# Performance work log

Hardware: AMD Instinct MI355X
Metric: run time of the kernel (lower is better)

The kernel has to match this reference:

```python
import jax, jax.numpy as jnp
import numpy as np

NEG_SLOPE = 0.2  # PyG GATConv default


def _gat_layer(x, src, dst, W, a_s, a_d, b, num_nodes):
    H, C = a_s.shape
    h = (x @ W).reshape(num_nodes, H, C)                     # [N,H,C]
    alpha_src = jnp.einsum('nhc,hc->nh', h, a_s)             # [N,H]
    alpha_dst = jnp.einsum('nhc,hc->nh', h, a_d)             # [N,H]
    e = jax.nn.leaky_relu(alpha_src[src] + alpha_dst[dst], NEG_SLOPE)  # [E,H]
    # segment softmax over incoming edges of each destination node
    m = jax.lax.stop_gradient(jax.ops.segment_max(e, dst, num_segments=num_nodes))
    e = jnp.exp(e - m[dst])
    den = jax.ops.segment_sum(e, dst, num_segments=num_nodes)
    alpha = e / den[dst]                                     # [E,H]
    msg = h[src] * alpha[:, :, None]                         # [E,H,C]
    out = jax.ops.segment_sum(msg, dst, num_segments=num_nodes)
    return out.reshape(num_nodes, H * C) + b


def setup_inputs() -> dict:
    key = jax.random.key(0)
    ks = jax.random.split(key, 10)
    N, E, D, H, C = 100000, 1600000, 128, 4, 32
    s = 1.0 / np.sqrt(D)
    return {
        'x': jax.random.normal(ks[0], (N, D), jnp.float32),
        'edge_index': jax.random.randint(ks[1], (2, E), 0, N, jnp.int64),
        'W1': jax.random.normal(ks[2], (D, H * C), jnp.float32) * s,
        'a_src1': jax.random.normal(ks[3], (H, C), jnp.float32) * s,
        'a_dst1': jax.random.normal(ks[4], (H, C), jnp.float32) * s,
        'b1': jnp.zeros((H * C,), jnp.float32),
        'W2': jax.random.normal(ks[5], (H * C, H * C), jnp.float32) * s,
        'a_src2': jax.random.normal(ks[6], (H, C), jnp.float32) * s,
        'a_dst2': jax.random.normal(ks[7], (H, C), jnp.float32) * s,
        'b2': jnp.zeros((H * C,), jnp.float32),
    }


def reference(x, edge_index, W1, a_src1, a_dst1, b1, W2, a_src2, a_dst2, b2):
    N = x.shape[0]
    loop = jnp.arange(N, dtype=edge_index.dtype)  # PyG add_self_loops=True
    src = jnp.concatenate([edge_index[0], loop])
    dst = jnp.concatenate([edge_index[1], loop])
    h = _gat_layer(x, src, dst, W1, a_src1, a_dst1, b1, N)
    h = jax.nn.relu(h)
    h = _gat_layer(h, src, dst, W2, a_src2, a_dst2, b2, N)
    return jax.nn.relu(h)
```

## Files before the change

kernel.cpp:

```cpp
#include <hip/hip_runtime.h>
#include <cstdint>
#include <cstddef>

#define NEG_SLOPE 0.2f
#define BIN_SHIFT 9
#define BCAP 16384
#define LOG2E 1.4426950408889634f

typedef short bf16x8 __attribute__((ext_vector_type(8)));
typedef float f32x4 __attribute__((ext_vector_type(4)));

#if __has_builtin(__builtin_amdgcn_exp2f)
#define EXP2(x) __builtin_amdgcn_exp2f(x)
#else
#define EXP2(x) exp2f(x)
#endif

static __device__ __forceinline__ unsigned short bf16r(float f) {
    unsigned u = __float_as_uint(f);
    return (unsigned short)((u + 0x7fffu + ((u >> 16) & 1u)) >> 16);
}
static __device__ __forceinline__ float bfu_lo(unsigned u) { return __uint_as_float(u << 16); }
static __device__ __forceinline__ float bfu_hi(unsigned u) { return __uint_as_float(u & 0xffff0000u); }

__global__ __launch_bounds__(256) void wprep_k(const float* __restrict__ W1, const float* __restrict__ W2,
                                               unsigned short* __restrict__ Wh1, unsigned short* __restrict__ Wl1,
                                               unsigned short* __restrict__ Wh2, unsigned short* __restrict__ Wl2,
                                               int* __restrict__ bcnt) {
    if (blockIdx.x == 0) bcnt[threadIdx.x] = 0;
    int t = blockIdx.x * 256 + threadIdx.x;
    const float* W;
    unsigned short *Wh, *Wl;
    int idx;
    if (t < 16384) { W = W1; Wh = Wh1; Wl = Wl1; idx = t; }
    else           { W = W2; Wh = Wh2; Wl = Wl2; idx = t - 16384; }
    int c = idx >> 7;
    int k = idx & 127;
    float w = W[(size_t)k * 128 + c];
    unsigned short h = bf16r(w);
    float lo = w - __uint_as_float((unsigned)h << 16);
    int dst = (k >> 5) * 4096 + (c >> 4) * 512 + (((k >> 3) & 3) * 16 + (c & 15)) * 8 + (k & 7);
    Wh[dst] = h;
    Wl[dst] = bf16r(lo);
}

__global__ __launch_bounds__(256) void bin_k(const int* __restrict__ srcI, const int* __restrict__ dstI,
                                             int E, int N, int K, int* __restrict__ bcnt,
                                             int* __restrict__ tmpE) {
    __shared__ int hist[256];
    __shared__ int lbase[256];
    __shared__ int lstart[256];
    __shared__ int cur[256];
    __shared__ int sc[256];
    __shared__ int staged[4096];
    __shared__ unsigned char bs[4096];
    const int t = threadIdx.x;
    const int M = E + N;
    const int chunk0 = blockIdx.x * 4096;
    hist[t] = 0;
    __syncthreads();

    int pk[16], bk[16];
#pragma unroll
    for (int j = 0; j < 16; ++j) {
        int i = chunk0 + t + j * 256;
        bk[j] = -1;
        if (i < M) {
            int ss, dd;
            if (i < E) { ss = srcI[i]; dd = dstI[i]; }
            else       { ss = i - E;  dd = ss; }
            if ((unsigned)dd < (unsigned)N && (unsigned)ss < (unsigned)N) {
                bk[j] = dd >> BIN_SHIFT;
                pk[j] = (ss << 9) | (dd & 511);
                atomicAdd(&hist[bk[j]], 1);
            }
        }
    }
    __syncthreads();
    const int h = hist[t];
    lbase[t] = (h > 0) ? atomicAdd(&bcnt[t], h) : 0;
    sc[t] = h;
    __syncthreads();
    for (int off = 1; off < 256; off <<= 1) {
        int v = (t >= off) ? sc[t - off] : 0;
        __syncthreads();
        sc[t] += v;
        __syncthreads();
    }
    lstart[t] = sc[t] - h;
    cur[t]    = sc[t] - h;
    __syncthreads();
#pragma unroll
    for (int j = 0; j < 16; ++j) {
        if (bk[j] >= 0) {
            int r = atomicAdd(&cur[bk[j]], 1);
            staged[r] = pk[j];
            bs[r] = (unsigned char)bk[j];
        }
    }
    const int total = sc[255];
    __syncthreads();
    for (int s = t; s < total; s += 256) {
        int b = bs[s];
        int posInBucket = lbase[b] + (s - lstart[b]);
        if (posInBucket < BCAP) tmpE[(size_t)b * BCAP + posInBucket] = staged[s];
    }
}

__global__ __launch_bounds__(256) void scatter_csr_k(const int* __restrict__ tmpE,
                                                     const int* __restrict__ bcnt,
                                                     int* __restrict__ rowptr,
                                                     int* __restrict__ colOff,
                                                     int N, int K) {
    __shared__ int pre[256];
    __shared__ int cur[512];
    __shared__ int ss[256];
    const int t = threadIdx.x;
    const int b = blockIdx.x;

    int bc = (t < K) ? min(bcnt[t], BCAP) : 0;
    pre[t] = bc;
    __syncthreads();
    for (int off = 1; off < 256; off <<= 1) {
        int v = (t >= off) ? pre[t - off] : 0;
        __syncthreads();
        pre[t] += v;
        __syncthreads();
    }
    const int base_b = (b == 0) ? 0 : pre[b - 1];
    const int cnt_b  = pre[b] - base_b;
    if (b == K - 1 && t == 0) rowptr[N] = pre[K - 1];

    const int nlo = b << BIN_SHIFT;
    const int nhi = min(nlo + (1 << BIN_SHIFT), N);
    const int nn  = nhi - nlo;
    const int* te = tmpE + (size_t)b * BCAP;

    cur[t] = 0;
    cur[t + 256] = 0;
    __syncthreads();
    for (int i = t; i < cnt_b; i += 256) atomicAdd(&cur[te[i] & 511], 1);
    __syncthreads();

    int v0 = cur[2 * t], v1 = cur[2 * t + 1];
    ss[t] = v0 + v1;
    __syncthreads();
    for (int off = 1; off < 256; off <<= 1) {
        int v = (t >= off) ? ss[t - off] : 0;
        __syncthreads();
        ss[t] += v;
        __syncthreads();
    }
    int e0 = (t == 0) ? 0 : ss[t - 1];
    int e1 = e0 + v0;
    if (2 * t < nn)     rowptr[nlo + 2 * t]     = base_b + e0;
    if (2 * t + 1 < nn) rowptr[nlo + 2 * t + 1] = base_b + e1;
    cur[2 * t] = e0;
    cur[2 * t + 1] = e1;
    __syncthreads();

    for (int i = t; i < cnt_b; i += 256) {
        int v = te[i];
        int r = atomicAdd(&cur[v & 511], 1);
        colOff[base_b + r] = ((unsigned)v >> 9) << 8;
    }
}

__global__ __launch_bounds__(256) void gemm_mfma_k(const float* __restrict__ X,
                                                   const unsigned short* __restrict__ Wh,
                                                   const unsigned short* __restrict__ Wl,
                                                   const float* __restrict__ a_s,
                                                   const float* __restrict__ a_d,
                                                   unsigned short* __restrict__ Hout,
                                                   float* __restrict__ asrc,
                                                   float* __restrict__ adst,
                                                   int N) {
    __shared__ __align__(16) unsigned short hstage[4][32][132];
    const int tid = threadIdx.x;
    const int wid = tid >> 6;
    const int l   = tid & 63;
    const int l15 = l & 15;
    const int lh  = l >> 4;
    const int waveRow = blockIdx.x * 128 + wid * 32;
    if (waveRow >= N) return;

    f32x4 acc[2][8];
#pragma unroll
    for (int m = 0; m < 2; ++m)
#pragma unroll
        for (int f = 0; f < 8; ++f)
#pragma unroll
            for (int c = 0; c < 4; ++c) acc[m][f][c] = 0.f;

    const int r0 = waveRow + l15;
    const int r1 = waveRow + 16 + l15;
    const size_t xoff0 = (size_t)min(r0, N - 1) * 128;
    const size_t xoff1 = (size_t)min(r1, N - 1) * 128;
    const int kb = lh * 8;

#pragma unroll
    for (int ks = 0; ks < 4; ++ks) {
        bf16x8 ah[2], al[2];
#pragma unroll
        for (int m = 0; m < 2; ++m) {
            const float* xp = X + (m ? xoff1 : xoff0) + ks * 32 + kb;
            float4 v0 = *(const float4*)xp;
            float4 v1 = *(const float4*)(xp + 4);
            float xs[8] = {v0.x, v0.y, v0.z, v0.w, v1.x, v1.y, v1.z, v1.w};
#pragma unroll
            for (int j = 0; j < 8; ++j) {
                unsigned short h = bf16r(xs[j]);
                float hf = __uint_as_float((unsigned)h << 16);
                ah[m][j] = (short)h;
                al[m][j] = (short)bf16r(xs[j] - hf);
            }
        }
        const unsigned short* wbh = Wh + ks * 4096 + l * 8;
        const unsigned short* wbl = Wl + ks * 4096 + l * 8;
#pragma unroll
        for (int f = 0; f < 8; ++f) {
            bf16x8 wh = *(const bf16x8*)(wbh + f * 512);
            bf16x8 wl = *(const bf16x8*)(wbl + f * 512);
#pragma unroll
            for (int m = 0; m < 2; ++m) {
                acc[m][f] = __builtin_amdgcn_mfma_f32_16x16x32_bf16(ah[m], wh, acc[m][f], 0, 0, 0);
                acc[m][f] = __builtin_amdgcn_mfma_f32_16x16x32_bf16(al[m], wh, acc[m][f], 0, 0, 0);
                acc[m][f] = __builtin_amdgcn_mfma_f32_16x16x32_bf16(ah[m], wl, acc[m][f], 0, 0, 0);
            }
        }
    }

    float asf[8], adf[8];
#pragma unroll
    for (int f = 0; f < 8; ++f) {
        asf[f] = a_s[f * 16 + l15];
        adf[f] = a_d[f * 16 + l15];
    }
    const int q = l15;
#pragma unroll
    for (int m = 0; m < 2; ++m) {
#pragma unroll
        for (int r = 0; r < 4; ++r) {
            float ps[4] = {0.f, 0.f, 0.f, 0.f};
            float pd[4] = {0.f, 0.f, 0.f, 0.f};
#pragma unroll
            for (int f = 0; f < 8; ++f) {
                float v = acc[m][f][r];
                ps[f >> 1] = fmaf(v, asf[f], ps[f >> 1]);
                pd[f >> 1] = fmaf(v, adf[f], pd[f >> 1]);
                hstage[wid][m * 16 + lh * 4 + r][f * 16 + l15] = bf16r(v);
            }
#pragma unroll
            for (int mask = 1; mask < 16; mask <<= 1) {
#pragma unroll
                for (int h = 0; h < 4; ++h) {
                    ps[h] += __shfl_xor(ps[h], mask);
                    pd[h] += __shfl_xor(pd[h], mask);
                }
            }
            int row = waveRow + m * 16 + lh * 4 + r;
            if (q < 8 && row < N) {
                float v0 = (q & 1) ? ps[1] : ps[0];
                float v1 = (q & 1) ? ps[3] : ps[2];
                float vs = (q & 2) ? v1 : v0;
                float w0 = (q & 1) ? pd[1] : pd[0];
                float w1 = (q & 1) ? pd[3] : pd[2];
                float vd = (q & 2) ? w1 : w0;
                if (q < 4) asrc[row * 4 + q] = vs * LOG2E;
                else       adst[row * 4 + (q - 4)] = vd * LOG2E;
            }
        }
    }

#pragma unroll
    for (int it = 0; it < 8; ++it) {
        int row = it * 4 + lh;
        const unsigned short* hp = &hstage[wid][row][l15 * 8];
        uint2 aa = *(const uint2*)hp;
        uint2 bb = *(const uint2*)(hp + 4);
        int grow = waveRow + row;
        if (grow < N) {
            uint4 o;
            o.x = aa.x; o.y = aa.y; o.z = bb.x; o.w = bb.y;
            *(uint4*)&Hout[(size_t)grow * 128 + l15 * 8] = o;
        }
    }
}

__global__ __launch_bounds__(256) void aggregate_k(const unsigned short* __restrict__ Hbuf,
                                                   const float* __restrict__ asrc,
                                                   const float* __restrict__ adst,
                                                   const int* __restrict__ rowptr,
                                                   const int* __restrict__ colOff,
                                                   const float* __restrict__ bias,
                                                   float* __restrict__ out, int N) {
    int wave = (blockIdx.x * 256 + threadIdx.x) >> 6;
    int lane = threadIdx.x & 63;
    if (wave >= N) return;
    const int n = wave;
    const int c0 = lane * 2;
    const int head = c0 >> 5;
    const float adh = adst[n * 4 + head];
    const char* Hb = (const char*)Hbuf;
    const char* As = (const char*)asrc;
    const int hoff = c0 * 2;
    const int aoff = head * 4;

    int b = __builtin_amdgcn_readfirstlane(rowptr[n]);
    int e = __builtin_amdgcn_readfirstlane(rowptr[n + 1]);
    float acc0 = 0.f, acc1 = 0.f, sw = 0.f;
    for (int p = b; p < e; p += 8) {
        int off[8];
#pragma unroll
        for (int j = 0; j < 8; ++j) off[j] = colOff[min(p + j, e - 1)];
        float a[8];
#pragma unroll
        for (int j = 0; j < 8; ++j) a[j] = *(const float*)(As + (off[j] >> 4) + aoff);
        unsigned hu[8];
#pragma unroll
        for (int j = 0; j < 8; ++j) hu[j] = *(const unsigned*)(Hb + off[j] + hoff);
#pragma unroll
        for (int j = 0; j < 8; ++j) {
            float x = a[j] + adh;
            float w = (p + j < e) ? EXP2(fmaxf(x, NEG_SLOPE * x)) : 0.f;
            sw += w;
            acc0 = fmaf(w, bfu_lo(hu[j]), acc0);
            acc1 = fmaf(w, bfu_hi(hu[j]), acc1);
        }
    }
    float inv = 1.f / sw;
    float o0 = fmaxf(acc0 * inv + bias[c0], 0.f);
    float o1 = fmaxf(acc1 * inv + bias[c0 + 1], 0.f);
    *(float2*)&out[(size_t)n * 128 + c0] = make_float2(o0, o1);
}


extern "C" void kernel_launch(void* const* d_in, const int* in_sizes, int n_in,
                              void* d_out, int out_size, void* d_ws, size_t ws_size,
                              hipStream_t stream) {
    const float* X   = (const float*)d_in[0];
    const int*   EI  = (const int*)d_in[1];
    const float* W1  = (const float*)d_in[2];
    const float* as1 = (const float*)d_in[3];
    const float* ad1 = (const float*)d_in[4];
    const float* b1  = (const float*)d_in[5];
    const float* W2  = (const float*)d_in[6];
    const float* as2 = (const float*)d_in[7];
    const float* ad2 = (const float*)d_in[8];
    const float* b2  = (const float*)d_in[9];

    const int N = in_sizes[0] / 128;
    const int E = in_sizes[1] / 2;
    const int M = E + N;
    const int K = (N + (1 << BIN_SHIFT) - 1) >> BIN_SHIFT;
    const int* srcI = EI;
    const int* dstI = EI + E;

    char* w = (char*)d_ws;
    auto alloc = [&](size_t bytes) {
        char* p = w;
        w += (bytes + 255) & ~(size_t)255;
        return p;
    };
    unsigned short* Hbuf = (unsigned short*)alloc((size_t)N * 128 * 2);
    float* asrc   = (float*)alloc((size_t)N * 4 * 4);
    float* adst   = (float*)alloc((size_t)N * 4 * 4);
    int*   rowptr = (int*)alloc((size_t)(N + 1) * 4);
    int*   colOff = (int*)alloc((size_t)M * 4);
    int*   tmpE   = (int*)alloc((size_t)K * BCAP * 4);
    int*   bcnt   = (int*)alloc(256 * 4);
    unsigned short* Wt1h = (unsigned short*)alloc(128 * 128 * 2);
    unsigned short* Wt1l = (unsigned short*)alloc(128 * 128 * 2);
    unsigned short* Wt2h = (unsigned short*)alloc(128 * 128 * 2);
    unsigned short* Wt2l = (unsigned short*)alloc(128 * 128 * 2);

    const int gemmBlocks = (N + 127) / 128;
    float* out = (float*)d_out;

    wprep_k<<<128, 256, 0, stream>>>(W1, W2, Wt1h, Wt1l, Wt2h, Wt2l, bcnt);
    bin_k<<<(M + 4095) / 4096, 256, 0, stream>>>(srcI, dstI, E, N, K, bcnt, tmpE);
    scatter_csr_k<<<K, 256, 0, stream>>>(tmpE, bcnt, rowptr, colOff, N, K);
    gemm_mfma_k<<<gemmBlocks, 256, 0, stream>>>(X, Wt1h, Wt1l, as1, ad1, Hbuf, asrc, adst, N);
    aggregate_k<<<((size_t)N * 64 + 255) / 256, 256, 0, stream>>>(Hbuf, asrc, adst, rowptr, colOff, b1, out, N);
    gemm_mfma_k<<<gemmBlocks, 256, 0, stream>>>(out, Wt2h, Wt2l, as2, ad2, Hbuf, asrc, adst, N);
    aggregate_k<<<((size_t)N * 64 + 255) / 256, 256, 0, stream>>>(Hbuf, asrc, adst, rowptr, colOff, b2, out, N);
}
```

Baseline: 378.3 us.

## Fuse pipeline stages into two persistent cooperative kernels with grid syncs

Replaces the seven separate launches with two cooperative persistent kernels. One does weight prep, binning and CSR scatter; the other does both GEMM and aggregation layers. Grid-wide syncs and threadfences replace kernel boundaries. This removes launch gaps and per-kernel tail effects, but the fixed grid size and the occupancy hint of 3 blocks per unit may lower parallelism or occupancy for the latency-bound aggregation. Grid-stride loops and the original multi-launch path are kept as a fallback if the cooperative launch fails.

```diff
diff --git a/kernel.cpp b/kernel.cpp
--- a/kernel.cpp
+++ b/kernel.cpp
@@ -1,6 +1,9 @@
 #include <hip/hip_runtime.h>
+#include <hip/hip_cooperative_groups.h>
 #include <cstdint>
 #include <cstddef>
+
+namespace cg = cooperative_groups;
 
 #define NEG_SLOPE 0.2f
 #define BIN_SHIFT 9
@@ -23,12 +26,10 @@
 static __device__ __forceinline__ float bfu_lo(unsigned u) { return __uint_as_float(u << 16); }
 static __device__ __forceinline__ float bfu_hi(unsigned u) { return __uint_as_float(u & 0xffff0000u); }
 
-__global__ __launch_bounds__(256) void wprep_k(const float* __restrict__ W1, const float* __restrict__ W2,
-                                               unsigned short* __restrict__ Wh1, unsigned short* __restrict__ Wl1,
-                                               unsigned short* __restrict__ Wh2, unsigned short* __restrict__ Wl2,
-                                               int* __restrict__ bcnt) {
-    if (blockIdx.x == 0) bcnt[threadIdx.x] = 0;
-    int t = blockIdx.x * 256 + threadIdx.x;
+
+static __device__ __forceinline__ void wprep_elem(int t, const float* W1, const float* W2,
+                                                  unsigned short* Wh1, unsigned short* Wl1,
+                                                  unsigned short* Wh2, unsigned short* Wl2) {
     const float* W;
     unsigned short *Wh, *Wl;
     int idx;
@@ -44,19 +45,13 @@
     Wl[dst] = bf16r(lo);
 }
 
-__global__ __launch_bounds__(256) void bin_k(const int* __restrict__ srcI, const int* __restrict__ dstI,
-                                             int E, int N, int K, int* __restrict__ bcnt,
-                                             int* __restrict__ tmpE) {
-    __shared__ int hist[256];
-    __shared__ int lbase[256];
-    __shared__ int lstart[256];
-    __shared__ int cur[256];
-    __shared__ int sc[256];
-    __shared__ int staged[4096];
-    __shared__ unsigned char bs[4096];
+static __device__ void bin_body(int bid, const int* __restrict__ srcI, const int* __restrict__ dstI,
+                                int E, int N, int K, int* __restrict__ bcnt, int* __restrict__ tmpE,
+                                int* hist, int* lbase, int* lstart, int* cur, int* sc,
+                                int* staged, unsigned char* bs) {
     const int t = threadIdx.x;
     const int M = E + N;
-    const int chunk0 = blockIdx.x * 4096;
+    const int chunk0 = bid * 4096;
     hist[t] = 0;
     __syncthreads();
 
@@ -105,18 +100,13 @@
         int posInBucket = lbase[b] + (s - lstart[b]);
         if (posInBucket < BCAP) tmpE[(size_t)b * BCAP + posInBucket] = staged[s];
     }
-}
-
-__global__ __launch_bounds__(256) void scatter_csr_k(const int* __restrict__ tmpE,
-                                                     const int* __restrict__ bcnt,
-                                                     int* __restrict__ rowptr,
-                                                     int* __restrict__ colOff,
-                                                     int N, int K) {
-    __shared__ int pre[256];
-    __shared__ int cur[512];
-    __shared__ int ss[256];
+    __syncthreads();
+}
+
+static __device__ void scatter_body(int b, const int* __restrict__ tmpE, const int* __restrict__ bcnt,
+                                    int* __restrict__ rowptr, int* __restrict__ colOff,
+                                    int N, int K, int* pre, int* cur, int* ss) {
     const int t = threadIdx.x;
-    const int b = blockIdx.x;
 
     int bc = (t < K) ? min(bcnt[t], BCAP) : 0;
     pre[t] = bc;
@@ -164,24 +154,24 @@
         int r = atomicAdd(&cur[v & 511], 1);
         colOff[base_b + r] = ((unsigned)v >> 9) << 8;
     }
-}
-
-__global__ __launch_bounds__(256) void gemm_mfma_k(const float* __restrict__ X,
-                                                   const unsigned short* __restrict__ Wh,
-                                                   const unsigned short* __restrict__ Wl,
-                                                   const float* __restrict__ a_s,
-                                                   const float* __restrict__ a_d,
-                                                   unsigned short* __restrict__ Hout,
-                                                   float* __restrict__ asrc,
-                                                   float* __restrict__ adst,
-                                                   int N) {
-    __shared__ __align__(16) unsigned short hstage[4][32][132];
+    __syncthreads();
+}
+
+static __device__ void gemm_body(int bid, const float* __restrict__ X,
+                                 const unsigned short* __restrict__ Wh,
+                                 const unsigned short* __restrict__ Wl,
+                                 const float* __restrict__ a_s,
+                                 const float* __restrict__ a_d,
+                                 unsigned short* __restrict__ Hout,
+                                 float* __restrict__ asrc,
+                                 float* __restrict__ adst,
+                                 int N, unsigned short* hstage) {
     const int tid = threadIdx.x;
     const int wid = tid >> 6;
     const int l   = tid & 63;
     const int l15 = l & 15;
     const int lh  = l >> 4;
-    const int waveRow = blockIdx.x * 128 + wid * 32;
+    const int waveRow = bid * 128 + wid * 32;
     if (waveRow >= N) return;
 
     f32x4 acc[2][8];
@@ -248,7 +238,7 @@
                 float v = acc[m][f][r];
                 ps[f >> 1] = fmaf(v, asf[f], ps[f >> 1]);
                 pd[f >> 1] = fmaf(v, adf[f], pd[f >> 1]);
-                hstage[wid][m * 16 + lh * 4 + r][f * 16 + l15] = bf16r(v);
+                hstage[((wid * 32) + m * 16 + lh * 4 + r) * 132 + f * 16 + l15] = bf16r(v);
             }
 #pragma unroll
             for (int mask = 1; mask < 16; mask <<= 1) {
@@ -275,7 +265,7 @@
 #pragma unroll
     for (int it = 0; it < 8; ++it) {
         int row = it * 4 + lh;
-        const unsigned short* hp = &hstage[wid][row][l15 * 8];
+        const unsigned short* hp = hstage + ((wid * 32) + row) * 132 + l15 * 8;
         uint2 aa = *(const uint2*)hp;
         uint2 bb = *(const uint2*)(hp + 4);
         int grow = waveRow + row;
@@ -287,17 +277,14 @@
     }
 }
 
-__global__ __launch_bounds__(256) void aggregate_k(const unsigned short* __restrict__ Hbuf,
-                                                   const float* __restrict__ asrc,
-                                                   const float* __restrict__ adst,
-                                                   const int* __restrict__ rowptr,
-                                                   const int* __restrict__ colOff,
-                                                   const float* __restrict__ bias,
-                                                   float* __restrict__ out, int N) {
-    int wave = (blockIdx.x * 256 + threadIdx.x) >> 6;
-    int lane = threadIdx.x & 63;
-    if (wave >= N) return;
-    const int n = wave;
+static __device__ void agg_body(int grp, const unsigned short* __restrict__ Hbuf,
+                                const float* __restrict__ asrc, const float* __restrict__ adst,
+                                const int* __restrict__ rowptr, const int* __restrict__ colOff,
+                                const float* __restrict__ bias, float* __restrict__ out, int N) {
+    const int wid  = threadIdx.x >> 6;
+    const int lane = threadIdx.x & 63;
+    const int n = grp * 4 + wid;
+    if (n >= N) return;
     const int c0 = lane * 2;
     const int head = c0 >> 5;
     const float adh = adst[n * 4 + head];
@@ -332,6 +319,111 @@
     float o0 = fmaxf(acc0 * inv + bias[c0], 0.f);
     float o1 = fmaxf(acc1 * inv + bias[c0 + 1], 0.f);
     *(float2*)&out[(size_t)n * 128 + c0] = make_float2(o0, o1);
+}
+
+
+struct PrepArgs {
+    const float *W1, *W2;
+    unsigned short *Wh1, *Wl1, *Wh2, *Wl2;
+    int* bcnt;
+    const int *srcI, *dstI;
+    int* tmpE;
+    int *rowptr, *colOff;
+    int E, N, K, nchunks;
+};
+
+__global__ __launch_bounds__(256) void prep_coop_k(PrepArgs a) {
+    __shared__ int hist[256], lbase[256], lstart[256], curA[256], sc[256];
+    __shared__ int staged[4096];
+    __shared__ unsigned char bs[4096];
+    __shared__ int pre[256], curB[512], ss[256];
+    cg::grid_group grid = cg::this_grid();
+    const int t = threadIdx.x;
+
+    if (blockIdx.x == 0) a.bcnt[t] = 0;
+    for (int i = blockIdx.x * 256 + t; i < 32768; i += gridDim.x * 256)
+        wprep_elem(i, a.W1, a.W2, a.Wh1, a.Wl1, a.Wh2, a.Wl2);
+    __threadfence();
+    grid.sync();
+
+    for (int c = blockIdx.x; c < a.nchunks; c += gridDim.x)
+        bin_body(c, a.srcI, a.dstI, a.E, a.N, a.K, a.bcnt, a.tmpE,
+                 hist, lbase, lstart, curA, sc, staged, bs);
+    __threadfence();
+    grid.sync();
+
+    for (int b = blockIdx.x; b < a.K; b += gridDim.x)
+        scatter_body(b, a.tmpE, a.bcnt, a.rowptr, a.colOff, a.N, a.K, pre, curB, ss);
+}
+
+struct MainArgs {
+    const float* X;
+    const unsigned short *Wh1, *Wl1, *Wh2, *Wl2;
+    const float *as1, *ad1, *b1, *as2, *ad2, *b2;
+    unsigned short* Hbuf;
+    float *asrc, *adst;
+    const int *rowptr, *colOff;
+    float* out;
+    int N, gemmTiles, nodeGroups;
+};
+
+__global__ __launch_bounds__(256, 3) void main_coop_k(MainArgs a) {
+    __shared__ __align__(16) unsigned short hstage[4 * 32 * 132];
+    cg::grid_group grid = cg::this_grid();
+
+    for (int tl = blockIdx.x; tl < a.gemmTiles; tl += gridDim.x)
+        gemm_body(tl, a.X, a.Wh1, a.Wl1, a.as1, a.ad1, a.Hbuf, a.asrc, a.adst, a.N, hstage);
+    __threadfence();
+    grid.sync();
+    for (int gp = blockIdx.x; gp < a.nodeGroups; gp += gridDim.x)
+        agg_body(gp, a.Hbuf, a.asrc, a.adst, a.rowptr, a.colOff, a.b1, a.out, a.N);
+    __threadfence();
+    grid.sync();
+    for (int tl = blockIdx.x; tl < a.gemmTiles; tl += gridDim.x)
+        gemm_body(tl, a.out, a.Wh2, a.Wl2, a.as2, a.ad2, a.Hbuf, a.asrc, a.adst, a.N, hstage);
+    __threadfence();
+    grid.sync();
+    for (int gp = blockIdx.x; gp < a.nodeGroups; gp += gridDim.x)
+        agg_body(gp, a.Hbuf, a.asrc, a.adst, a.rowptr, a.colOff, a.b2, a.out, a.N);
+}
+
+
+__global__ __launch_bounds__(256) void wprep_k(const float* W1, const float* W2,
+                                               unsigned short* Wh1, unsigned short* Wl1,
+                                               unsigned short* Wh2, unsigned short* Wl2,
+                                               int* bcnt) {
+    if (blockIdx.x == 0) bcnt[threadIdx.x] = 0;
+    int t = blockIdx.x * 256 + threadIdx.x;
+    if (t < 32768) wprep_elem(t, W1, W2, Wh1, Wl1, Wh2, Wl2);
+}
+
+__global__ __launch_bounds__(256) void bin_k(const int* srcI, const int* dstI,
+                                             int E, int N, int K, int* bcnt, int* tmpE) {
+    __shared__ int hist[256], lbase[256], lstart[256], curA[256], sc[256];
+    __shared__ int staged[4096];
+    __shared__ unsigned char bs[4096];
+    bin_body(blockIdx.x, srcI, dstI, E, N, K, bcnt, tmpE, hist, lbase, lstart, curA, sc, staged, bs);
+}
+
+__global__ __launch_bounds__(256) void scatter_csr_k(const int* tmpE, const int* bcnt,
+                                                     int* rowptr, int* colOff, int N, int K) {
+    __shared__ int pre[256], curB[512], ss[256];
+    scatter_body(blockIdx.x, tmpE, bcnt, rowptr, colOff, N, K, pre, curB, ss);
+}
+
+__global__ __launch_bounds__(256) void gemm_mfma_k(const float* X, const unsigned short* Wh,
+                                                   const unsigned short* Wl, const float* a_s,
+                                                   const float* a_d, unsigned short* Hout,
+                                                   float* asrc, float* adst, int N) {
+    __shared__ __align__(16) unsigned short hstage[4 * 32 * 132];
+    gemm_body(blockIdx.x, X, Wh, Wl, a_s, a_d, Hout, asrc, adst, N, hstage);
+}
+
+__global__ __launch_bounds__(256) void aggregate_k(const unsigned short* Hbuf, const float* asrc,
+                                                   const float* adst, const int* rowptr,
+                                                   const int* colOff, const float* bias,
+                                                   float* out, int N) {
+    agg_body(blockIdx.x, Hbuf, asrc, adst, rowptr, colOff, bias, out, N);
 }
 
 
@@ -374,14 +466,70 @@
     unsigned short* Wt2h = (unsigned short*)alloc(128 * 128 * 2);
     unsigned short* Wt2l = (unsigned short*)alloc(128 * 128 * 2);
 
-    const int gemmBlocks = (N + 127) / 128;
+    const int gemmTiles  = (N + 127) / 128;
+    const int nodeGroups = (N + 3) / 4;
+    const int nchunks    = (M + 4095) / 4096;
     float* out = (float*)d_out;
 
-    wprep_k<<<128, 256, 0, stream>>>(W1, W2, Wt1h, Wt1l, Wt2h, Wt2l, bcnt);
-    bin_k<<<(M + 4095) / 4096, 256, 0, stream>>>(srcI, dstI, E, N, K, bcnt, tmpE);
-    scatter_csr_k<<<K, 256, 0, stream>>>(tmpE, bcnt, rowptr, colOff, N, K);
-    gemm_mfma_k<<<gemmBlocks, 256, 0, stream>>>(X, Wt1h, Wt1l, as1, ad1, Hbuf, asrc, adst, N);
-    aggregate_k<<<((size_t)N * 64 + 255) / 256, 256, 0, stream>>>(Hbuf, asrc, adst, rowptr, colOff, b1, out, N);
-    gemm_mfma_k<<<gemmBlocks, 256, 0, stream>>>(out, Wt2h, Wt2l, as2, ad2, Hbuf, asrc, adst, N);
-    aggregate_k<<<((size_t)N * 64 + 255) / 256, 256, 0, stream>>>(Hbuf, asrc, adst, rowptr, colOff, b2, out, N);
-}
+    static int s_numCU = 0, s_prepOcc = 0, s_mainOcc = 0;
+    if (s_numCU == 0) {
+        int dev = 0;
+        hipDeviceProp_t props;
+        if (hipGetDevice(&dev) == hipSuccess && hipGetDeviceProperties(&props, dev) == hipSuccess)
+            s_numCU = props.multiProcessorCount;
+        if (s_numCU <= 0) s_numCU = 256;
+        if (hipOccupancyMaxActiveBlocksPerMultiprocessor(&s_prepOcc, prep_coop_k, 256, 0) != hipSuccess)
+            s_prepOcc = 0;
+        if (hipOccupancyMaxActiveBlocksPerMultiprocessor(&s_mainOcc, main_coop_k, 256, 0) != hipSuccess)
+            s_mainOcc = 0;
+        (void)hipGetLastError();
+    }
+
+    bool prepDone = false, mainDone = false;
+
+    if (s_prepOcc > 0) {
+        int prepGrid = s_prepOcc * s_numCU;
+        if (prepGrid > nchunks) prepGrid = nchunks;
+        PrepArgs pa;
+        pa.W1 = W1; pa.W2 = W2;
+        pa.Wh1 = Wt1h; pa.Wl1 = Wt1l; pa.Wh2 = Wt2h; pa.Wl2 = Wt2l;
+        pa.bcnt = bcnt; pa.srcI = srcI; pa.dstI = dstI; pa.tmpE = tmpE;
+        pa.rowptr = rowptr; pa.colOff = colOff;
+        pa.E = E; pa.N = N; pa.K = K; pa.nchunks = nchunks;
+        void* pargs[] = { &pa };
+        if (hipLaunchCooperativeKernel(prep_coop_k, dim3(prepGrid), dim3(256), pargs, 0, stream) == hipSuccess)
+            prepDone = true;
+        else
+            (void)hipGetLastError();
+    }
+    if (!prepDone) {
+        wprep_k<<<128, 256, 0, stream>>>(W1, W2, Wt1h, Wt1l, Wt2h, Wt2l, bcnt);
+        bin_k<<<nchunks, 256, 0, stream>>>(srcI, dstI, E, N, K, bcnt, tmpE);
+        scatter_csr_k<<<K, 256, 0, stream>>>(tmpE, bcnt, rowptr, colOff, N, K);
+    }
+
+    if (s_mainOcc > 0) {
+        int mainGrid = s_mainOcc * s_numCU;
+        if (mainGrid > nodeGroups) mainGrid = nodeGroups;
+        MainArgs ma;
+        ma.X = X;
+        ma.Wh1 = Wt1h; ma.Wl1 = Wt1l; ma.Wh2 = Wt2h; ma.Wl2 = Wt2l;
+        ma.as1 = as1; ma.ad1 = ad1; ma.b1 = b1;
+        ma.as2 = as2; ma.ad2 = ad2; ma.b2 = b2;
+        ma.Hbuf = Hbuf; ma.asrc = asrc; ma.adst = adst;
+        ma.rowptr = rowptr; ma.colOff = colOff;
+        ma.out = out;
+        ma.N = N; ma.gemmTiles = gemmTiles; ma.nodeGroups = nodeGroups;
+        void* margs[] = { &ma };
+        if (hipLaunchCooperativeKernel(main_coop_k, dim3(mainGrid), dim3(256), margs, 0, stream) == hipSuccess)
+            mainDone = true;
+        else
+            (void)hipGetLastError();
+    }
+    if (!mainDone) {
+        gemm_mfma_k<<<gemmTiles, 256, 0, stream>>>(X, Wt1h, Wt1l, as1, ad1, Hbuf, asrc, adst, N);
+        aggregate_k<<<nodeGroups, 256, 0, stream>>>(Hbuf, asrc, adst, rowptr, colOff, b1, out, N);
+        gemm_mfma_k<<<gemmTiles, 256, 0, stream>>>(out, Wt2h, Wt2l, as2, ad2, Hbuf, asrc, adst, N);
+        aggregate_k<<<nodeGroups, 256, 0, stream>>>(Hbuf, asrc, adst, rowptr, colOff, b2, out, N);
+    }
+}
```

Measured after the change: 622.2 us. +64.5%, slower.

## Merge independent prep and layer-1 GEMM with CSR scatter into shared launches

Applied to the files above, without the earlier changes.

Weight preparation and edge binning now run as different block ranges of one kernel, and the CSR scatter runs alongside the first-layer GEMM in another combined kernel, since neither pair depends on the other. This removes two kernel launches and lets independent work overlap on the GPU. The bucket counter reset moves to a hipMemsetAsync. The combined kernels carry the larger shared-memory footprint and register use of their heavier half, which may lower occupancy for the lighter half.

```diff
diff --git a/kernel.cpp b/kernel.cpp
--- a/kernel.cpp
+++ b/kernel.cpp
@@ -23,12 +23,10 @@
 static __device__ __forceinline__ float bfu_lo(unsigned u) { return __uint_as_float(u << 16); }
 static __device__ __forceinline__ float bfu_hi(unsigned u) { return __uint_as_float(u & 0xffff0000u); }
 
-__global__ __launch_bounds__(256) void wprep_k(const float* __restrict__ W1, const float* __restrict__ W2,
-                                               unsigned short* __restrict__ Wh1, unsigned short* __restrict__ Wl1,
-                                               unsigned short* __restrict__ Wh2, unsigned short* __restrict__ Wl2,
-                                               int* __restrict__ bcnt) {
-    if (blockIdx.x == 0) bcnt[threadIdx.x] = 0;
-    int t = blockIdx.x * 256 + threadIdx.x;
+
+static __device__ __forceinline__ void wprep_elem(int t, const float* W1, const float* W2,
+                                                  unsigned short* Wh1, unsigned short* Wl1,
+                                                  unsigned short* Wh2, unsigned short* Wl2) {
     const float* W;
     unsigned short *Wh, *Wl;
     int idx;
@@ -44,19 +42,13 @@
     Wl[dst] = bf16r(lo);
 }
 
-__global__ __launch_bounds__(256) void bin_k(const int* __restrict__ srcI, const int* __restrict__ dstI,
-                                             int E, int N, int K, int* __restrict__ bcnt,
-                                             int* __restrict__ tmpE) {
-    __shared__ int hist[256];
-    __shared__ int lbase[256];
-    __shared__ int lstart[256];
-    __shared__ int cur[256];
-    __shared__ int sc[256];
-    __shared__ int staged[4096];
-    __shared__ unsigned char bs[4096];
+static __device__ void bin_body(int bid, const int* __restrict__ srcI, const int* __restrict__ dstI,
+                                int E, int N, int K, int* __restrict__ bcnt, int* __restrict__ tmpE,
+                                int* hist, int* lbase, int* lstart, int* cur, int* sc,
+                                int* staged, unsigned char* bs) {
     const int t = threadIdx.x;
     const int M = E + N;
-    const int chunk0 = blockIdx.x * 4096;
+    const int chunk0 = bid * 4096;
     hist[t] = 0;
     __syncthreads();
 
@@ -107,16 +99,10 @@
     }
 }
 
-__global__ __launch_bounds__(256) void scatter_csr_k(const int* __restrict__ tmpE,
-                                                     const int* __restrict__ bcnt,
-                                                     int* __restrict__ rowptr,
-                                                     int* __restrict__ colOff,
-                                                     int N, int K) {
-    __shared__ int pre[256];
-    __shared__ int cur[512];
-    __shared__ int ss[256];
+static __device__ void scatter_body(int b, const int* __restrict__ tmpE, const int* __restrict__ bcnt,
+                                    int* __restrict__ rowptr, int* __restrict__ colOff,
+                                    int N, int K, int* pre, int* cur, int* ss) {
     const int t = threadIdx.x;
-    const int b = blockIdx.x;
 
     int bc = (t < K) ? min(bcnt[t], BCAP) : 0;
     pre[t] = bc;
@@ -166,22 +152,21 @@
     }
 }
 
-__global__ __launch_bounds__(256) void gemm_mfma_k(const float* __restrict__ X,
-                                                   const unsigned short* __restrict__ Wh,
-                                                   const unsigned short* __restrict__ Wl,
-                                                   const float* __restrict__ a_s,
-                                                   const float* __restrict__ a_d,
-                                                   unsigned short* __restrict__ Hout,
-                                                   float* __restrict__ asrc,
-                                                   float* __restrict__ adst,
-                                                   int N) {
-    __shared__ __align__(16) unsigned short hstage[4][32][132];
+static __device__ void gemm_body(int bid, const float* __restrict__ X,
+                                 const unsigned short* __restrict__ Wh,
+                                 const unsigned short* __restrict__ Wl,
+                                 const float* __restrict__ a_s,
+                                 const float* __restrict__ a_d,
+                                 unsigned short* __restrict__ Hout,
+                                 float* __restrict__ asrc,
+                                 float* __restrict__ adst,
+                                 int N, unsigned short* hstage) {
     const int tid = threadIdx.x;
     const int wid = tid >> 6;
     const int l   = tid & 63;
     const int l15 = l & 15;
     const int lh  = l >> 4;
-    const int waveRow = blockIdx.x * 128 + wid * 32;
+    const int waveRow = bid * 128 + wid * 32;
     if (waveRow >= N) return;
 
     f32x4 acc[2][8];
@@ -248,7 +233,7 @@
                 float v = acc[m][f][r];
                 ps[f >> 1] = fmaf(v, asf[f], ps[f >> 1]);
                 pd[f >> 1] = fmaf(v, adf[f], pd[f >> 1]);
-                hstage[wid][m * 16 + lh * 4 + r][f * 16 + l15] = bf16r(v);
+                hstage[((wid * 32) + m * 16 + lh * 4 + r) * 132 + f * 16 + l15] = bf16r(v);
             }
 #pragma unroll
             for (int mask = 1; mask < 16; mask <<= 1) {
@@ -275,7 +260,7 @@
 #pragma unroll
     for (int it = 0; it < 8; ++it) {
         int row = it * 4 + lh;
-        const unsigned short* hp = &hstage[wid][row][l15 * 8];
+        const unsigned short* hp = hstage + ((wid * 32) + row) * 132 + l15 * 8;
         uint2 aa = *(const uint2*)hp;
         uint2 bb = *(const uint2*)(hp + 4);
         int grow = waveRow + row;
@@ -287,6 +272,109 @@
     }
 }
 
+static __device__ void agg_body(int grp, const unsigned short* __restrict__ Hbuf,
+                                const float* __restrict__ asrc, const float* __restrict__ adst,
+                                const int* __restrict__ rowptr, const int* __restrict__ colOff,
+                                const float* __restrict__ bias, float* __restrict__ out, int N) {
+    const int wid  = threadIdx.x >> 6;
+    const int lane = threadIdx.x & 63;
+    const int n = grp * 4 + wid;
+    if (n >= N) return;
+    const int c0 = lane * 2;
+    const int head = c0 >> 5;
+    const float adh = adst[n * 4 + head];
+    const char* Hb = (const char*)Hbuf;
+    const char* As = (const char*)asrc;
+    const int hoff = c0 * 2;
+    const int aoff = head * 4;
+
+    int b = __builtin_amdgcn_readfirstlane(rowptr[n]);
+    int e = __builtin_amdgcn_readfirstlane(rowptr[n + 1]);
+    float acc0 = 0.f, acc1 = 0.f, sw = 0.f;
+    for (int p = b; p < e; p += 8) {
+        int off[8];
+#pragma unroll
+        for (int j = 0; j < 8; ++j) off[j] = colOff[min(p + j, e - 1)];
+        float a[8];
+#pragma unroll
+        for (int j = 0; j < 8; ++j) a[j] = *(const float*)(As + (off[j] >> 4) + aoff);
+        unsigned hu[8];
+#pragma unroll
+        for (int j = 0; j < 8; ++j) hu[j] = *(const unsigned*)(Hb + off[j] + hoff);
+#pragma unroll
+        for (int j = 0; j < 8; ++j) {
+            float x = a[j] + adh;
+            float w = (p + j < e) ? EXP2(fmaxf(x, NEG_SLOPE * x)) : 0.f;
+            sw += w;
+            acc0 = fmaf(w, bfu_lo(hu[j]), acc0);
+            acc1 = fmaf(w, bfu_hi(hu[j]), acc1);
+        }
+    }
+    float inv = 1.f / sw;
+    float o0 = fmaxf(acc0 * inv + bias[c0], 0.f);
+    float o1 = fmaxf(acc1 * inv + bias[c0 + 1], 0.f);
+    *(float2*)&out[(size_t)n * 128 + c0] = make_float2(o0, o1);
+}
+
+
+__global__ __launch_bounds__(256) void prep1_k(const float* __restrict__ W1, const float* __restrict__ W2,
+                                               unsigned short* __restrict__ Wh1, unsigned short* __restrict__ Wl1,
+                                               unsigned short* __restrict__ Wh2, unsigned short* __restrict__ Wl2,
+                                               const int* __restrict__ srcI, const int* __restrict__ dstI,
+                                               int E, int N, int K, int* __restrict__ bcnt,
+                                               int* __restrict__ tmpE) {
+    __shared__ int hist[256], lbase[256], lstart[256], curA[256], sc[256];
+    __shared__ int staged[4096];
+    __shared__ unsigned char bs[4096];
+    const int bid = blockIdx.x;
+    if (bid < 128) {
+        int t = bid * 256 + threadIdx.x;
+        wprep_elem(t, W1, W2, Wh1, Wl1, Wh2, Wl2);
+    } else {
+        bin_body(bid - 128, srcI, dstI, E, N, K, bcnt, tmpE,
+                 hist, lbase, lstart, curA, sc, staged, bs);
+    }
+}
+
+__global__ __launch_bounds__(256) void gemm1_scatter_k(const int* __restrict__ tmpE,
+                                                       const int* __restrict__ bcnt,
+                                                       int* __restrict__ rowptr,
+                                                       int* __restrict__ colOff,
+                                                       int K,
+                                                       const float* __restrict__ X,
+                                                       const unsigned short* __restrict__ Wh,
+                                                       const unsigned short* __restrict__ Wl,
+                                                       const float* __restrict__ a_s,
+                                                       const float* __restrict__ a_d,
+                                                       unsigned short* __restrict__ Hout,
+                                                       float* __restrict__ asrc,
+                                                       float* __restrict__ adst,
+                                                       int N) {
+    __shared__ __align__(16) unsigned short smem[4 * 32 * 132];
+    const int bid = blockIdx.x;
+    if (bid < K) {
+        int* pre = (int*)smem;
+        int* cur = pre + 256;
+        int* ss  = cur + 512;
+        scatter_body(bid, tmpE, bcnt, rowptr, colOff, N, K, pre, cur, ss);
+    } else {
+        gemm_body(bid - K, X, Wh, Wl, a_s, a_d, Hout, asrc, adst, N, smem);
+    }
+}
+
+__global__ __launch_bounds__(256) void gemm_mfma_k(const float* __restrict__ X,
+                                                   const unsigned short* __restrict__ Wh,
+                                                   const unsigned short* __restrict__ Wl,
+                                                   const float* __restrict__ a_s,
+                                                   const float* __restrict__ a_d,
+                                                   unsigned short* __restrict__ Hout,
+                                                   float* __restrict__ asrc,
+                                                   float* __restrict__ adst,
+                                                   int N) {
+    __shared__ __align__(16) unsigned short hstage[4 * 32 * 132];
+    gemm_body(blockIdx.x, X, Wh, Wl, a_s, a_d, Hout, asrc, adst, N, hstage);
+}
+
 __global__ __launch_bounds__(256) void aggregate_k(const unsigned short* __restrict__ Hbuf,
                                                    const float* __restrict__ asrc,
                                                    const float* __restrict__ adst,
@@ -294,44 +382,7 @@
                                                    const int* __restrict__ colOff,
                                                    const float* __restrict__ bias,
                                                    float* __restrict__ out, int N) {
-    int wave = (blockIdx.x * 256 + threadIdx.x) >> 6;
-    int lane = threadIdx.x & 63;
-    if (wave >= N) return;
-    const int n = wave;
-    const int c0 = lane * 2;
-    const int head = c0 >> 5;
-    const float adh = adst[n * 4 + head];
-    const char* Hb = (const char*)Hbuf;
-    const char* As = (const char*)asrc;
-    const int hoff = c0 * 2;
-    const int aoff = head * 4;
-
-    int b = __builtin_amdgcn_readfirstlane(rowptr[n]);
-    int e = __builtin_amdgcn_readfirstlane(rowptr[n + 1]);
-    float acc0 = 0.f, acc1 = 0.f, sw = 0.f;
-    for (int p = b; p < e; p += 8) {
-        int off[8];
-#pragma unroll
-        for (int j = 0; j < 8; ++j) off[j] = colOff[min(p + j, e - 1)];
-        float a[8];
-#pragma unroll
-        for (int j = 0; j < 8; ++j) a[j] = *(const float*)(As + (off[j] >> 4) + aoff);
-        unsigned hu[8];
-#pragma unroll
-        for (int j = 0; j < 8; ++j) hu[j] = *(const unsigned*)(Hb + off[j] + hoff);
-#pragma unroll
-        for (int j = 0; j < 8; ++j) {
-            float x = a[j] + adh;
-            float w = (p + j < e) ? EXP2(fmaxf(x, NEG_SLOPE * x)) : 0.f;
-            sw += w;
-            acc0 = fmaf(w, bfu_lo(hu[j]), acc0);
-            acc1 = fmaf(w, bfu_hi(hu[j]), acc1);
-        }
-    }
-    float inv = 1.f / sw;
-    float o0 = fmaxf(acc0 * inv + bias[c0], 0.f);
-    float o1 = fmaxf(acc1 * inv + bias[c0 + 1], 0.f);
-    *(float2*)&out[(size_t)n * 128 + c0] = make_float2(o0, o1);
+    agg_body(blockIdx.x, Hbuf, asrc, adst, rowptr, colOff, bias, out, N);
 }
 
 
@@ -374,14 +425,17 @@
     unsigned short* Wt2h = (unsigned short*)alloc(128 * 128 * 2);
     unsigned short* Wt2l = (unsigned short*)alloc(128 * 128 * 2);
 
-    const int gemmBlocks = (N + 127) / 128;
+    const int gemmTiles  = (N + 127) / 128;
+    const int nodeGroups = (N + 3) / 4;
+    const int nchunks    = (M + 4095) / 4096;
     float* out = (float*)d_out;
 
-    wprep_k<<<128, 256, 0, stream>>>(W1, W2, Wt1h, Wt1l, Wt2h, Wt2l, bcnt);
-    bin_k<<<(M + 4095) / 4096, 256, 0, stream>>>(srcI, dstI, E, N, K, bcnt, tmpE);
-    scatter_csr_k<<<K, 256, 0, stream>>>(tmpE, bcnt, rowptr, colOff, N, K);
-    gemm_mfma_k<<<gemmBlocks, 256, 0, stream>>>(X, Wt1h, Wt1l, as1, ad1, Hbuf, asrc, adst, N);
-    aggregate_k<<<((size_t)N * 64 + 255) / 256, 256, 0, stream>>>(Hbuf, asrc, adst, rowptr, colOff, b1, out, N);
-    gemm_mfma_k<<<gemmBlocks, 256, 0, stream>>>(out, Wt2h, Wt2l, as2, ad2, Hbuf, asrc, adst, N);
-    aggregate_k<<<((size_t)N * 64 + 255) / 256, 256, 0, stream>>>(Hbuf, asrc, adst, rowptr, colOff, b2, out, N);
-}
+    hipMemsetAsync(bcnt, 0, 256 * 4, stream);
+    prep1_k<<<128 + nchunks, 256, 0, stream>>>(W1, W2, Wt1h, Wt1l, Wt2h, Wt2l,
+                                               srcI, dstI, E, N, K, bcnt, tmpE);
+    gemm1_scatter_k<<<K + gemmTiles, 256, 0, stream>>>(tmpE, bcnt, rowptr, colOff, K,
+                                                       X, Wt1h, Wt1l, as1, ad1, Hbuf, asrc, adst, N);
+    aggregate_k<<<nodeGroups, 256, 0, stream>>>(Hbuf, asrc, adst, rowptr, colOff, b1, out, N);
+    gemm_mfma_k<<<gemmTiles, 256, 0, stream>>>(out, Wt2h, Wt2l, as2, ad2, Hbuf, asrc, adst, N);
+    aggregate_k<<<nodeGroups, 256, 0, stream>>>(Hbuf, asrc, adst, rowptr, colOff, b2, out, N);
+}
```

Result: slower. 405.5 us (+7.2%).
